# Performance work log

Measured on AMD Instinct MI355X. Metric: run time of the kernel, lower is better.

The kernel has to match this reference:

```python
import jax, jax.numpy as jnp
import numpy as np

TOP_K = 2
AUX_COEFF = 0.01

def setup_inputs() -> dict:
    key = jax.random.key(0)
    k1, k2, k3, k4 = jax.random.split(key, 4)
    B, T, d, E = 4, 1024, 1024, 8
    x = jax.random.normal(k1, (B, T, d), dtype=jnp.float32)
    w_gate = jax.random.normal(k2, (d, E), dtype=jnp.float32) * 0.02
    w1 = jax.random.normal(k3, (E, d, 4 * d), dtype=jnp.float32) * 0.02
    w2 = jax.random.normal(k4, (E, 4 * d, d), dtype=jnp.float32) * 0.02
    return {"x": x, "w_gate": w_gate, "w1": w1, "w2": w2}

def reference(x, w_gate, w1, w2):
    B, T, d = x.shape
    E = w_gate.shape[1]
    N = B * T
    xf = x.reshape(N, d)

    # Router: softmax over experts, top-k, renormalize
    logits = xf @ w_gate                      # [N, E]
    probs = jax.nn.softmax(logits, axis=-1)   # [N, E]
    topk_p, topk_i = jax.lax.top_k(probs, TOP_K)
    topk_p = topk_p / topk_p.sum(axis=-1, keepdims=True)

    # Combine weights: scatter top-k probs into [N, E] (equiv. to masked scatter-add loop)
    comb = jnp.zeros((N, E), dtype=x.dtype).at[
        jnp.arange(N)[:, None], topk_i].add(topk_p)

    # Grouped expert MLP (dense over experts, weighted combine)
    h = jnp.einsum('nd,edf->enf', xf, w1)     # [E, N, 4d]
    h = jax.nn.gelu(h, approximate=False)     # exact erf GELU like nn.GELU
    y = jnp.einsum('enf,efd->end', h, w2)     # [E, N, d]
    out = jnp.einsum('ne,end->nd', comb, y).reshape(B, T, d)

    # Load-balancing aux loss (training branch)
    counts = jnp.zeros((E,), dtype=x.dtype).at[topk_i.reshape(-1)].add(1.0)
    f = counts / (N * TOP_K)
    p = probs.mean(axis=0)
    aux_loss = AUX_COEFF * E * jnp.sum(f * p)
    return out, aux_loss
```

## Files before the change

kernel.cpp:

```cpp
#include <hip/hip_runtime.h>
#include <cmath>

#define N_TOK 4096
#define DDIM 1024
#define FDIM 4096
#define NEXP 8
#define MAXT 72
#define MAXROWS (MAXT * 128)

typedef __attribute__((ext_vector_type(4))) float f32x4;
typedef __attribute__((ext_vector_type(8))) __bf16 bf16x8;
typedef __attribute__((ext_vector_type(4))) unsigned short us4;
typedef __attribute__((ext_vector_type(8))) unsigned short us8;

__device__ __forceinline__ unsigned short f2bf(float f) {
  unsigned u = __builtin_bit_cast(unsigned, f);
  u += 0x7FFFu + ((u >> 16) & 1u);
  return (unsigned short)(u >> 16);
}

__device__ __forceinline__ void gload16(const void* g, void* l) {
  __builtin_amdgcn_global_load_lds(
      (const __attribute__((address_space(1))) unsigned int*)g,
      (__attribute__((address_space(3))) unsigned int*)l, 16, 0, 0);
}

__device__ __forceinline__ int xcd_remap(int h, int nwg) {
  int q = nwg >> 3, r = nwg & 7;
  int xcd = h & 7, o = h >> 3;
  return (xcd < r ? xcd * (q + 1) : r * (q + 1) + (xcd - r) * q) + o;
}

__global__ __launch_bounds__(64) void router_kernel(
    const float* __restrict__ x, const float* __restrict__ wg,
    float* __restrict__ probs, int* __restrict__ eids, float* __restrict__ ewts) {
  int n = blockIdx.x;
  int t = threadIdx.x;
  const float* xr = x + (size_t)n * DDIM;
  float acc[8] = {0, 0, 0, 0, 0, 0, 0, 0};
  for (int k = t; k < DDIM; k += 64) {
    float xv = xr[k];
    const float* wr = wg + k * 8;
#pragma unroll
    for (int e = 0; e < 8; e++) acc[e] = fmaf(xv, wr[e], acc[e]);
  }
#pragma unroll
  for (int off = 32; off > 0; off >>= 1) {
#pragma unroll
    for (int e = 0; e < 8; e++) acc[e] += __shfl_xor(acc[e], off, 64);
  }
  if (t == 0) {
    float mx = acc[0];
#pragma unroll
    for (int e = 1; e < 8; e++) mx = fmaxf(mx, acc[e]);
    float p[8], s = 0.f;
#pragma unroll
    for (int e = 0; e < 8; e++) { p[e] = expf(acc[e] - mx); s += p[e]; }
    float inv = 1.f / s;
#pragma unroll
    for (int e = 0; e < 8; e++) { p[e] *= inv; probs[n * 8 + e] = p[e]; }
    int i0 = 0;
#pragma unroll
    for (int e = 1; e < 8; e++) if (p[e] > p[i0]) i0 = e;
    int i1 = (i0 == 0) ? 1 : 0;
#pragma unroll
    for (int e = 0; e < 8; e++) if (e != i0 && p[e] > p[i1]) i1 = e;
    float sw = p[i0] + p[i1];
    eids[n * 2] = i0; eids[n * 2 + 1] = i1;
    ewts[n * 2] = p[i0] / sw; ewts[n * 2 + 1] = p[i1] / sw;
  }
}

__global__ __launch_bounds__(256) void plan_kernel(
    const float* __restrict__ probs, const int* __restrict__ eids,
    float* __restrict__ aux_out, int* __restrict__ meta) {
  __shared__ float pl[256][8];
  __shared__ int cl[256][8];
  __shared__ float ps2[8];
  __shared__ int cn2[8];
  int t = threadIdx.x;
  float pa[8] = {0, 0, 0, 0, 0, 0, 0, 0};
  int ca[8] = {0, 0, 0, 0, 0, 0, 0, 0};
  for (int n = t; n < N_TOK; n += 256) {
#pragma unroll
    for (int e = 0; e < 8; e++) pa[e] += probs[n * 8 + e];
    ca[eids[n * 2]]++; ca[eids[n * 2 + 1]]++;
  }
#pragma unroll
  for (int e = 0; e < 8; e++) { pl[t][e] = pa[e]; cl[t][e] = ca[e]; }
  __syncthreads();
  if (t < 8) {
    float s = 0; int c = 0;
    for (int i = 0; i < 256; i++) { s += pl[i][t]; c += cl[i][t]; }
    ps2[t] = s; cn2[t] = c;
  }
  __syncthreads();
  if (t == 0) {
    int tb = 0; float aux = 0.f;
    for (int e = 0; e < 8; e++) {
      int c = cn2[e];
      meta[e] = c; meta[8 + e] = 0; meta[16 + e] = tb;
      int tiles = (c + 127) >> 7;
      for (int i = 0; i < tiles; i++) meta[24 + tb + i] = e;
      tb += tiles;
      aux += ((float)c / (float)(N_TOK * 2)) * (ps2[e] / (float)N_TOK);
    }
    meta[96] = tb;
    *aux_out = 0.01f * 8.f * aux;
  }
}

__global__ __launch_bounds__(256) void scatter_kernel(
    const int* __restrict__ eids, int* __restrict__ meta,
    int* __restrict__ perm, int* __restrict__ inv) {
  int n = blockIdx.x * 256 + threadIdx.x;
  if (n >= N_TOK) return;
#pragma unroll
  for (int s = 0; s < 2; s++) {
    int e = eids[n * 2 + s];
    int pos = atomicAdd(&meta[8 + e], 1);
    int row = (meta[16 + e] << 7) + pos;
    perm[row] = n;
    inv[n * 2 + s] = row;
  }
}

__global__ __launch_bounds__(256) void convert_x_kernel(
    const float* __restrict__ x, unsigned short* __restrict__ xb) {
  int i = blockIdx.x * 256 + threadIdx.x;
  f32x4 v = ((const f32x4*)x)[i];
  us4 o = {f2bf(v[0]), f2bf(v[1]), f2bf(v[2]), f2bf(v[3])};
  ((us4*)xb)[i] = o;
}

__global__ __launch_bounds__(256) void transpose_conv(
    const float* __restrict__ src, unsigned short* __restrict__ dst, int R, int C) {
  __shared__ unsigned short tile[64 * 64];
  size_t eoff = (size_t)blockIdx.z * (size_t)R * (size_t)C;
  src += eoff; dst += eoff;
  int c0 = blockIdx.x << 6, r0 = blockIdx.y << 6;
  int t = threadIdx.x;
  int rl = (t >> 4) << 2;
  int cl = (t & 15) << 2;
  f32x4 v[4];
#pragma unroll
  for (int i = 0; i < 4; i++)
    v[i] = *(const f32x4*)(src + (size_t)(r0 + rl + i) * C + c0 + cl);
#pragma unroll
  for (int u = 0; u < 4; u++) {
    int c = cl + u;
    us4 o = {f2bf(v[0][u]), f2bf(v[1][u]), f2bf(v[2][u]), f2bf(v[3][u])};
    unsigned byteoff = (unsigned)c * 128 + ((((unsigned)(rl >> 3)) ^ (unsigned)(c & 7)) << 4) + (unsigned)(rl & 7) * 2;
    *(us4*)((char*)tile + byteoff) = o;
  }
  __syncthreads();
#pragma unroll
  for (int p = 0; p < 2; p++) {
    int id = t + p * 256;
    int c = id >> 3, q = id & 7;
    unsigned byteoff = (unsigned)c * 128 + (((unsigned)q ^ (unsigned)(c & 7)) << 4);
    us8 val = *(const us8*)((const char*)tile + byteoff);
    *(us8*)(dst + (size_t)(c0 + c) * R + r0 + q * 8) = val;
  }
}

template <int K, int NPANELS, bool GATHER, int MODE>
__global__ __launch_bounds__(256, 2) void gemm_kernel(
    const unsigned short* __restrict__ A,
    const unsigned short* __restrict__ Bt,
    unsigned short* __restrict__ Hout,
    float* __restrict__ Out,
    const int* __restrict__ perm,
    const int* __restrict__ tileExpert, const int* __restrict__ totalTiles,
    int NB) {
  __shared__ unsigned short ldsA[128 * 64];
  __shared__ unsigned short ldsB[128 * 64];
  constexpr int NWG = MAXT * NPANELS;
  int L = xcd_remap((int)blockIdx.x, NWG);
  int sup = L >> 5, wi = L & 31;
  constexpr int GM = MAXT / 8;
  int gm = sup % GM, gn = sup / GM;
  int tile = gm * 8 + (wi & 7);
  int nt = gn * 4 + (wi >> 3);
  if (tile >= *totalTiles) return;
  int e = tileExpert[tile];
  int m0 = tile << 7;
  int n0 = nt << 7;
  const unsigned short* Bbase = Bt + ((size_t)e * NB + n0) * K;
  int t = threadIdx.x;
  int wave = t >> 6, lane = t & 63;
  int g = lane >> 4, ln = lane & 15;
  int wm = wave >> 1, wn = wave & 1;

  const unsigned short* srcA[4];
  const unsigned short* srcB[4];
#pragma unroll
  for (int i = 0; i < 4; i++) {
    int c = wave * 256 + i * 64 + lane;
    int r = c >> 3, kc = c & 7;
    int rowA = GATHER ? perm[m0 + r] : (m0 + r);
    srcA[i] = A + (size_t)rowA * K + ((kc ^ (r & 7)) << 3);
    srcB[i] = Bbase + (size_t)r * K + ((kc ^ (r & 7)) << 3);
  }

  f32x4 acc[4][4];
#pragma unroll
  for (int a = 0; a < 4; a++)
#pragma unroll
    for (int b = 0; b < 4; b++) acc[a][b] = (f32x4){0.f, 0.f, 0.f, 0.f};

  for (int k0 = 0; k0 < K; k0 += 64) {
#pragma unroll
    for (int i = 0; i < 4; i++) {
      int cb = wave * 256 + i * 64;
      gload16(srcA[i] + k0, &ldsA[cb * 8]);
      gload16(srcB[i] + k0, &ldsB[cb * 8]);
    }
    __syncthreads();
#pragma unroll
    for (int ks = 0; ks < 2; ks++) {
      bf16x8 af[4], bfr[4];
      int q = ks * 4 + g;
#pragma unroll
      for (int mf = 0; mf < 4; mf++) {
        int m = wm * 64 + mf * 16 + ln;
        af[mf] = *(const bf16x8*)((const char*)ldsA + m * 128 + ((q ^ (m & 7)) << 4));
      }
#pragma unroll
      for (int nf = 0; nf < 4; nf++) {
        int n = wn * 64 + nf * 16 + ln;
        bfr[nf] = *(const bf16x8*)((const char*)ldsB + n * 128 + ((q ^ (n & 7)) << 4));
      }
#pragma unroll
      for (int mf = 0; mf < 4; mf++)
#pragma unroll
        for (int nf = 0; nf < 4; nf++)
          acc[mf][nf] = __builtin_amdgcn_mfma_f32_16x16x32_bf16(af[mf], bfr[nf], acc[mf][nf], 0, 0, 0);
    }
    __syncthreads();
  }

  if (MODE == 1) {
#pragma unroll
    for (int mf = 0; mf < 4; mf++) {
#pragma unroll
      for (int r = 0; r < 4; r++) {
        int row = m0 + wm * 64 + mf * 16 + g * 4 + r;
        unsigned short* hp = Hout + (size_t)row * NB + n0 + wn * 64 + ln;
#pragma unroll
        for (int nf = 0; nf < 4; nf++) {
          float v = acc[mf][nf][r];
          v = 0.5f * v * (1.f + erff(v * 0.70710678118654752f));
          hp[nf * 16] = f2bf(v);
        }
      }
    }
  } else {
#pragma unroll
    for (int mf = 0; mf < 4; mf++) {
#pragma unroll
      for (int r = 0; r < 4; r++) {
        int row = m0 + wm * 64 + mf * 16 + g * 4 + r;
        float* yp = Out + (size_t)row * NB + n0 + wn * 64 + ln;
#pragma unroll
        for (int nf = 0; nf < 4; nf++) yp[nf * 16] = acc[mf][nf][r];
      }
    }
  }
}

__global__ __launch_bounds__(256) void combine_kernel(
    const float* __restrict__ yscr, const int* __restrict__ inv,
    const float* __restrict__ ewts, float* __restrict__ out) {
  int n = blockIdx.x, t = threadIdx.x;
  int r0 = inv[n * 2], r1 = inv[n * 2 + 1];
  float w0 = ewts[n * 2], w1 = ewts[n * 2 + 1];
  f32x4 a = *(const f32x4*)(yscr + (size_t)r0 * DDIM + t * 4);
  f32x4 b = *(const f32x4*)(yscr + (size_t)r1 * DDIM + t * 4);
  f32x4 o;
#pragma unroll
  for (int j = 0; j < 4; j++) o[j] = w0 * a[j] + w1 * b[j];
  *(f32x4*)(out + (size_t)n * DDIM + t * 4) = o;
}

extern "C" void kernel_launch(void* const* d_in, const int* in_sizes, int n_in,
                              void* d_out, int out_size, void* d_ws, size_t ws_size,
                              hipStream_t stream) {
  const float* x = (const float*)d_in[0];
  const float* wgate = (const float*)d_in[1];
  const float* w1 = (const float*)d_in[2];
  const float* w2 = (const float*)d_in[3];
  float* out = (float*)d_out;

  char* w = (char*)d_ws;
  float* probs = (float*)w;                 w += (size_t)N_TOK * 8 * 4;
  int* eids = (int*)w;                      w += (size_t)N_TOK * 2 * 4;
  float* ewts = (float*)w;                  w += (size_t)N_TOK * 2 * 4;
  int* meta = (int*)w;                      w += 512;
  int* perm = (int*)w;                      w += (size_t)MAXROWS * 4;
  int* inv = (int*)w;                       w += (size_t)N_TOK * 2 * 4;
  unsigned short* xb = (unsigned short*)w;  w += (size_t)N_TOK * DDIM * 2;
  unsigned short* w1t = (unsigned short*)w; w += (size_t)NEXP * DDIM * FDIM * 2;
  unsigned short* w2t = (unsigned short*)w; w += (size_t)NEXP * DDIM * FDIM * 2;
  unsigned short* h = (unsigned short*)w;   w += (size_t)MAXROWS * FDIM * 2;
  float* yscr = (float*)w1t;

  hipMemsetAsync(perm, 0, (size_t)MAXROWS * 4, stream);

  router_kernel<<<N_TOK, 64, 0, stream>>>(x, wgate, probs, eids, ewts);
  plan_kernel<<<1, 256, 0, stream>>>(probs, eids, out + 4194304, meta);
  scatter_kernel<<<16, 256, 0, stream>>>(eids, meta, perm, inv);
  convert_x_kernel<<<4096, 256, 0, stream>>>(x, xb);
  transpose_conv<<<dim3(64, 16, 8), 256, 0, stream>>>(w1, w1t, DDIM, FDIM);
  transpose_conv<<<dim3(16, 64, 8), 256, 0, stream>>>(w2, w2t, FDIM, DDIM);
  gemm_kernel<DDIM, 32, true, 1><<<MAXT * 32, 256, 0, stream>>>(
      xb, w1t, h, nullptr, perm, meta + 24, meta + 96, FDIM);
  gemm_kernel<FDIM, 8, false, 2><<<MAXT * 8, 256, 0, stream>>>(
      h, w2t, nullptr, yscr, perm, meta + 24, meta + 96, DDIM);
  combine_kernel<<<N_TOK, 256, 0, stream>>>(yscr, inv, ewts, out);
}
```

Baseline: 385.3 us.

## Double-buffer LDS tiles to overlap global loads with MFMA compute

Replaces the single-buffered K loop, which had two barriers per step, with ping-pong LDS buffers. The next K-slice is issued with global_load_lds while MFMAs run on the current buffer, leaving one barrier per step. This doubles LDS use to 64 KB per block, which may limit the two-blocks-per-CU occupancy, and the stage is issued after the first fragment reads.

```diff
diff --git a/kernel.cpp b/kernel.cpp
--- a/kernel.cpp
+++ b/kernel.cpp
@@ -164,6 +164,44 @@
   }
 }
 
+
+#define STAGE_DB(NA, NB_, ko)                                                  \
+  _Pragma("unroll") for (int i = 0; i < 4; i++) {                              \
+    gload16(srcA[i] + (ko), (char*)(NA) + ldsoff[i]);                          \
+    gload16(srcB[i] + (ko), (char*)(NB_) + ldsoff[i]);                         \
+  }
+
+#define BODY_DB(CA, CB, NA, NB_, ko, dostage)                                  \
+  {                                                                            \
+    bf16x8 af[4], bfr[4];                                                      \
+    _Pragma("unroll") for (int mf = 0; mf < 4; mf++) {                         \
+      int m = wm * 64 + mf * 16 + ln;                                          \
+      af[mf] = *(const bf16x8*)((const char*)(CA) + m * 128 + ((g ^ (m & 7)) << 4)); \
+    }                                                                          \
+    _Pragma("unroll") for (int nf = 0; nf < 4; nf++) {                         \
+      int n = wn * 64 + nf * 16 + ln;                                          \
+      bfr[nf] = *(const bf16x8*)((const char*)(CB) + n * 128 + ((g ^ (n & 7)) << 4)); \
+    }                                                                          \
+    if (dostage) { STAGE_DB(NA, NB_, ko) }                                     \
+    _Pragma("unroll") for (int mf = 0; mf < 4; mf++)                           \
+    _Pragma("unroll") for (int nf = 0; nf < 4; nf++)                           \
+      acc[mf][nf] = __builtin_amdgcn_mfma_f32_16x16x32_bf16(                   \
+          af[mf], bfr[nf], acc[mf][nf], 0, 0, 0);                              \
+    _Pragma("unroll") for (int mf = 0; mf < 4; mf++) {                         \
+      int m = wm * 64 + mf * 16 + ln;                                          \
+      af[mf] = *(const bf16x8*)((const char*)(CA) + m * 128 + (((4 ^ g) ^ (m & 7)) << 4)); \
+    }                                                                          \
+    _Pragma("unroll") for (int nf = 0; nf < 4; nf++) {                         \
+      int n = wn * 64 + nf * 16 + ln;                                          \
+      bfr[nf] = *(const bf16x8*)((const char*)(CB) + n * 128 + (((4 ^ g) ^ (n & 7)) << 4)); \
+    }                                                                          \
+    _Pragma("unroll") for (int mf = 0; mf < 4; mf++)                           \
+    _Pragma("unroll") for (int nf = 0; nf < 4; nf++)                           \
+      acc[mf][nf] = __builtin_amdgcn_mfma_f32_16x16x32_bf16(                   \
+          af[mf], bfr[nf], acc[mf][nf], 0, 0, 0);                              \
+    __syncthreads();                                                           \
+  }
+
 template <int K, int NPANELS, bool GATHER, int MODE>
 __global__ __launch_bounds__(256, 2) void gemm_kernel(
     const unsigned short* __restrict__ A,
@@ -173,8 +211,13 @@
     const int* __restrict__ perm,
     const int* __restrict__ tileExpert, const int* __restrict__ totalTiles,
     int NB) {
-  __shared__ unsigned short ldsA[128 * 64];
-  __shared__ unsigned short ldsB[128 * 64];
+  constexpr int NT = K / 64;
+  static_assert(NT % 2 == 0, "NT even");
+  __shared__ unsigned short ldsA0[8192];
+  __shared__ unsigned short ldsB0[8192];
+  __shared__ unsigned short ldsA1[8192];
+  __shared__ unsigned short ldsB1[8192];
+
   constexpr int NWG = MAXT * NPANELS;
   int L = xcd_remap((int)blockIdx.x, NWG);
   int sup = L >> 5, wi = L & 31;
@@ -194,6 +237,7 @@
 
   const unsigned short* srcA[4];
   const unsigned short* srcB[4];
+  unsigned ldsoff[4];
 #pragma unroll
   for (int i = 0; i < 4; i++) {
     int c = wave * 256 + i * 64 + lane;
@@ -201,6 +245,7 @@
     int rowA = GATHER ? perm[m0 + r] : (m0 + r);
     srcA[i] = A + (size_t)rowA * K + ((kc ^ (r & 7)) << 3);
     srcB[i] = Bbase + (size_t)r * K + ((kc ^ (r & 7)) << 3);
+    ldsoff[i] = (unsigned)(wave * 256 + i * 64) * 16u;
   }
 
   f32x4 acc[4][4];
@@ -209,35 +254,14 @@
 #pragma unroll
     for (int b = 0; b < 4; b++) acc[a][b] = (f32x4){0.f, 0.f, 0.f, 0.f};
 
-  for (int k0 = 0; k0 < K; k0 += 64) {
-#pragma unroll
-    for (int i = 0; i < 4; i++) {
-      int cb = wave * 256 + i * 64;
-      gload16(srcA[i] + k0, &ldsA[cb * 8]);
-      gload16(srcB[i] + k0, &ldsB[cb * 8]);
-    }
-    __syncthreads();
-#pragma unroll
-    for (int ks = 0; ks < 2; ks++) {
-      bf16x8 af[4], bfr[4];
-      int q = ks * 4 + g;
-#pragma unroll
-      for (int mf = 0; mf < 4; mf++) {
-        int m = wm * 64 + mf * 16 + ln;
-        af[mf] = *(const bf16x8*)((const char*)ldsA + m * 128 + ((q ^ (m & 7)) << 4));
-      }
-#pragma unroll
-      for (int nf = 0; nf < 4; nf++) {
-        int n = wn * 64 + nf * 16 + ln;
-        bfr[nf] = *(const bf16x8*)((const char*)ldsB + n * 128 + ((q ^ (n & 7)) << 4));
-      }
-#pragma unroll
-      for (int mf = 0; mf < 4; mf++)
-#pragma unroll
-        for (int nf = 0; nf < 4; nf++)
-          acc[mf][nf] = __builtin_amdgcn_mfma_f32_16x16x32_bf16(af[mf], bfr[nf], acc[mf][nf], 0, 0, 0);
-    }
-    __syncthreads();
+  STAGE_DB(ldsA0, ldsB0, 0)
+  __syncthreads();
+
+#pragma unroll 1
+  for (int p = 0; p < NT / 2; ++p) {
+    int k1 = (2 * p + 1) * 64, k2 = (2 * p + 2) * 64;
+    BODY_DB(ldsA0, ldsB0, ldsA1, ldsB1, k1, true)
+    BODY_DB(ldsA1, ldsB1, ldsA0, ldsB0, k2, (2 * p + 2) < NT)
   }
 
   if (MODE == 1) {
```

New measurement: 430.4 us. 11.7% more time.
